# Performance work log

Hardware: AMD Instinct MI355X
Metric: run time of the kernel (lower is better)

The kernel has to match this reference:

```python
import jax, jax.numpy as jnp
import numpy as np

N, E = 50000, 800000
IN, HID, OUT = 256, 128, 128


def setup_inputs() -> dict:
    key = jax.random.key(0)
    ks = jax.random.split(key, 6)
    x = jax.random.normal(ks[0], (N, IN), dtype=jnp.float32)
    edge_index = jax.random.randint(ks[1], (2, E), 0, N, dtype=jnp.int32)
    # xavier_normal-ish scales (exact init values irrelevant for correctness baseline)
    W1 = jax.random.normal(ks[2], (IN, HID), dtype=jnp.float32) * (1.414 / np.sqrt(IN))
    att_src = jax.random.normal(ks[3], (HID,), dtype=jnp.float32) * 0.1
    att_dst = jax.random.normal(ks[4], (HID,), dtype=jnp.float32) * 0.1
    W2 = jax.random.normal(ks[5], (HID, OUT), dtype=jnp.float32) * (1.414 / np.sqrt(HID))
    return {"x": x, "edge_index": edge_index, "W1": W1,
            "att_src": att_src, "att_dst": att_dst, "W2": W2}


def _gat_layer(x, edge_index, W, a_src, a_dst):
    """GATConv(heads=1, concat=False, add_self_loops=False, dropout=0), attention=True."""
    n = x.shape[0]
    src, dst = edge_index[0], edge_index[1]  # message x_j = h[src], grouped by index = dst
    h = x @ W                                 # (N, C)
    e_src = h @ a_src                         # (N,) per-node attention logits
    e_dst = h @ a_dst                         # (N,)
    # per-edge: sigmoid(alpha_j + alpha_i), then scatter-softmax over dst neighborhoods
    alpha = jax.nn.sigmoid(e_src[src] + e_dst[dst])             # (E,)
    m = jax.ops.segment_max(alpha, dst, num_segments=n)          # stable softmax max
    ex = jnp.exp(alpha - m[dst])
    denom = jax.ops.segment_sum(ex, dst, num_segments=n)
    w = ex / denom[dst]                                          # (E,)
    # scatter-add aggregation of weighted source features; heads=1 so mean over heads is identity
    return jax.ops.segment_sum(h[src] * w[:, None], dst, num_segments=n)  # (N, C)


def reference(x, edge_index, W1, att_src, att_dst, W2):
    h1 = jax.nn.elu(_gat_layer(x, edge_index, W1, att_src, att_dst))
    # conv2 called with attention=False: mm(h1, W2).view(N,1,C).mean(1) == plain linear
    return h1 @ W2
```

## Files before the change

### kernel.cpp

```cpp
#include <hip/hip_runtime.h>
#include <hip/hip_bf16.h>

#define N_NODES 50000
#define N_EDGES 800000
#define DIN 256
#define DHID 128
#define DOUT 128
#define NBUCK 196
#define BINBLK 256
#define EPB 3125
#define G1TILES 391

typedef __attribute__((ext_vector_type(8))) short bf16x8;
typedef __attribute__((ext_vector_type(4))) float f32x4;

__device__ inline unsigned short f2b(float f) {
    __hip_bfloat16 b = __float2bfloat16(f);
    return *reinterpret_cast<unsigned short*>(&b);
}

__global__ __launch_bounds__(1024) void convW_lhist_kernel(
    const float* __restrict__ W1, const float* __restrict__ W2,
    const int* __restrict__ ei,
    unsigned short* __restrict__ W1t, unsigned short* __restrict__ W2t,
    int* __restrict__ blockHist)
{
    __shared__ int h[NBUCK];
    const int blk = blockIdx.x;
    const int tid = threadIdx.x;

    if (blk < 48) {
        int i = blk * 1024 + tid;
        if (i < DIN * DHID) {
            int n = i >> 8, k = i & 255;
            int kt = k >> 5, q = (k >> 3) & 3, e = k & 7;
            int t = n >> 4, m = n & 15;
            W1t[(((kt * 8 + t) * 64) + (q * 16 + m)) * 8 + e] = f2b(W1[k * DHID + n]);
        } else {
            int j = i - DIN * DHID;
            int n = j >> 7, k = j & 127;
            int kt = k >> 5, q = (k >> 3) & 3, e = k & 7;
            int t = n >> 4, m = n & 15;
            W2t[(((kt * 8 + t) * 64) + (q * 16 + m)) * 8 + e] = f2b(W2[k * DOUT + n]);
        }
        return;
    }

    const int b = blk - 48;
    if (tid < NBUCK) h[tid] = 0;
    __syncthreads();
    const int base = b * EPB;
    #pragma unroll 1
    for (int it = 0; it < 4; ++it) {
        int e = base + it * 1024 + tid;
        if (e < base + EPB)
            atomicAdd(&h[ei[N_EDGES + e] >> 8], 1);
    }
    __syncthreads();
    if (tid < NBUCK) blockHist[tid * 256 + b] = h[tid];
}

__global__ __launch_bounds__(256) void gemm1_scan_kernel(
    const float* __restrict__ x,
    const unsigned short* __restrict__ W1t,
    const float* __restrict__ att_src,
    const float* __restrict__ att_dst,
    const int* __restrict__ blockHist,
    unsigned short* __restrict__ hb,
    float* __restrict__ es,
    float* __restrict__ ed,
    int* __restrict__ matrixScan)
{
    __shared__ int bs[256];
    __shared__ int sc[256];
    const int tid = threadIdx.x;

    if (blockIdx.x >= G1TILES) {
        const int b = blockIdx.x - G1TILES;

        int tot = 0;
        if (tid < NBUCK) {
            const int* row = blockHist + tid * 256;
            #pragma unroll 4
            for (int i = 0; i < 256; ++i) tot += row[i];
        }
        bs[tid] = tot;
        __syncthreads();
        #pragma unroll
        for (int off = 1; off < 256; off <<= 1) {
            int u = (tid >= off) ? bs[tid - off] : 0;
            __syncthreads();
            bs[tid] += u;
            __syncthreads();
        }
        const int base = (b == 0) ? 0 : bs[b - 1];

        int c = blockHist[b * 256 + tid];
        sc[tid] = c;
        __syncthreads();
        #pragma unroll
        for (int off = 1; off < 256; off <<= 1) {
            int u = (tid >= off) ? sc[tid - off] : 0;
            __syncthreads();
            sc[tid] += u;
            __syncthreads();
        }
        matrixScan[b * 256 + tid] = base + sc[tid] - c;
        return;
    }

    const int wave = tid >> 6, lane = tid & 63;
    const int row0 = blockIdx.x * 128 + wave * 32;
    const int m = lane & 15, q = lane >> 4;

    int r0 = row0 + m;
    int r1 = row0 + 16 + m;
    int rc0 = (r0 < N_NODES) ? r0 : 0;
    int rc1 = (r1 < N_NODES) ? r1 : 0;

    f32x4 acc0[8], acc1[8];
    #pragma unroll
    for (int t = 0; t < 8; ++t) {
        acc0[t] = (f32x4){0.f, 0.f, 0.f, 0.f};
        acc1[t] = (f32x4){0.f, 0.f, 0.f, 0.f};
    }

    const float* xr0 = x + (size_t)rc0 * DIN + q * 8;
    const float* xr1 = x + (size_t)rc1 * DIN + q * 8;
    const short* wb  = (const short*)W1t + lane * 8;

    #pragma unroll
    for (int kt = 0; kt < 8; ++kt) {
        float4 f0 = *(const float4*)(xr0 + kt * 32);
        float4 f1 = *(const float4*)(xr0 + kt * 32 + 4);
        float4 g0 = *(const float4*)(xr1 + kt * 32);
        float4 g1 = *(const float4*)(xr1 + kt * 32 + 4);
        bf16x8 a0, a1;
        a0[0] = (short)f2b(f0.x); a0[1] = (short)f2b(f0.y);
        a0[2] = (short)f2b(f0.z); a0[3] = (short)f2b(f0.w);
        a0[4] = (short)f2b(f1.x); a0[5] = (short)f2b(f1.y);
        a0[6] = (short)f2b(f1.z); a0[7] = (short)f2b(f1.w);
        a1[0] = (short)f2b(g0.x); a1[1] = (short)f2b(g0.y);
        a1[2] = (short)f2b(g0.z); a1[3] = (short)f2b(g0.w);
        a1[4] = (short)f2b(g1.x); a1[5] = (short)f2b(g1.y);
        a1[6] = (short)f2b(g1.z); a1[7] = (short)f2b(g1.w);
        #pragma unroll
        for (int t = 0; t < 8; ++t) {
            bf16x8 b = *(const bf16x8*)(wb + (kt * 8 + t) * 512);
            acc0[t] = __builtin_amdgcn_mfma_f32_16x16x32_bf16(a0, b, acc0[t], 0, 0, 0);
            acc1[t] = __builtin_amdgcn_mfma_f32_16x16x32_bf16(a1, b, acc1[t], 0, 0, 0);
        }
    }

    #pragma unroll
    for (int reg = 0; reg < 4; ++reg) {
        int ra = row0 + q * 4 + reg;
        int rb = row0 + 16 + q * 4 + reg;
        if (ra < N_NODES) {
            #pragma unroll
            for (int t = 0; t < 8; ++t)
                hb[(size_t)ra * DHID + t * 16 + m] = f2b(acc0[t][reg]);
        }
        if (rb < N_NODES) {
            #pragma unroll
            for (int t = 0; t < 8; ++t)
                hb[(size_t)rb * DHID + t * 16 + m] = f2b(acc1[t][reg]);
        }
    }

    float es0[4] = {0,0,0,0}, ed0[4] = {0,0,0,0};
    float es1[4] = {0,0,0,0}, ed1[4] = {0,0,0,0};
    #pragma unroll
    for (int t = 0; t < 8; ++t) {
        float as = att_src[t * 16 + m];
        float ad = att_dst[t * 16 + m];
        #pragma unroll
        for (int reg = 0; reg < 4; ++reg) {
            es0[reg] += acc0[t][reg] * as;
            ed0[reg] += acc0[t][reg] * ad;
            es1[reg] += acc1[t][reg] * as;
            ed1[reg] += acc1[t][reg] * ad;
        }
    }
    #pragma unroll
    for (int off = 8; off; off >>= 1)
        #pragma unroll
        for (int reg = 0; reg < 4; ++reg) {
            es0[reg] += __shfl_xor(es0[reg], off);
            ed0[reg] += __shfl_xor(ed0[reg], off);
            es1[reg] += __shfl_xor(es1[reg], off);
            ed1[reg] += __shfl_xor(ed1[reg], off);
        }
    if (m == 0) {
        #pragma unroll
        for (int reg = 0; reg < 4; ++reg) {
            int ra = row0 + q * 4 + reg;
            int rb = row0 + 16 + q * 4 + reg;
            if (ra < N_NODES) { es[ra] = es0[reg]; ed[ra] = ed0[reg]; }
            if (rb < N_NODES) { es[rb] = es1[reg]; ed[rb] = ed1[reg]; }
        }
    }
}

__global__ __launch_bounds__(1024) void binpass_kernel(
    const int* __restrict__ ei,
    const float* __restrict__ es,
    const float* __restrict__ ed,
    const int* __restrict__ matrixScan,
    int2* __restrict__ binned)
{
    __shared__ int lcur[NBUCK];
    const int t = threadIdx.x, blk = blockIdx.x;
    if (t < NBUCK) lcur[t] = matrixScan[t * 256 + blk];
    __syncthreads();
    const int base = blk * EPB;
    #pragma unroll 1
    for (int it = 0; it < 4; ++it) {
        int e = base + it * 1024 + t;
        if (e < base + EPB) {
            int s = ei[e];
            int d = ei[N_EDGES + e];
            float a  = es[s] + ed[d];
            float sg = 1.f / (1.f + __expf(-a));
            float w  = __expf(sg);
            int pos = atomicAdd(&lcur[d >> 8], 1);
            binned[pos] = make_int2(s | ((d & 255) << 16), __float_as_int(w));
        }
    }
}

__global__ __launch_bounds__(1024) void sortpass_kernel(
    const int2* __restrict__ binned,
    const int* __restrict__ matrixScan,
    int2* __restrict__ sortedSW,
    int* __restrict__ offset,
    int* __restrict__ count)
{
    __shared__ int lhist[256], lscan[256], lcur[256];
    const int t = threadIdx.x, b = blockIdx.x;
    const int start = matrixScan[b * 256];
    const int end   = (b == NBUCK - 1) ? N_EDGES : matrixScan[(b + 1) * 256];
    const int cnt   = end - start;

    if (t < 256) lhist[t] = 0;
    __syncthreads();
    for (int i = t; i < cnt; i += 1024)
        atomicAdd(&lhist[(binned[start + i].x >> 16) & 255], 1);
    __syncthreads();

    int v = 0;
    if (t < 256) { v = lhist[t]; lscan[t] = v; }
    __syncthreads();
    #pragma unroll
    for (int off = 1; off < 256; off <<= 1) {
        int u = 0;
        if (t < 256 && t >= off) u = lscan[t - off];
        __syncthreads();
        if (t < 256) lscan[t] += u;
        __syncthreads();
    }
    if (t < 256) {
        int excl = lscan[t] - v;
        int node = (b << 8) + t;
        if (node < N_NODES) { offset[node] = start + excl; count[node] = v; }
        lcur[t] = excl;
    }
    __syncthreads();

    for (int i = t; i < cnt; i += 1024) {
        int2 ent = binned[start + i];
        int dlow = (ent.x >> 16) & 255;
        int pos = atomicAdd(&lcur[dlow], 1);
        sortedSW[start + pos] = make_int2(ent.x & 0xFFFF, ent.y);
    }
}

__global__ __launch_bounds__(256) void agg_kernel(
    const int2* __restrict__ sortedSW,
    const int* __restrict__ offset,
    const int* __restrict__ count,
    const unsigned short* __restrict__ hb,
    unsigned int* __restrict__ h1b)
{
    int node = (blockIdx.x * 256 + threadIdx.x) >> 6;
    int lane = threadIdx.x & 63;
    if (node >= N_NODES) return;

    int beg = offset[node];
    int deg = count[node];

    float2 acc = make_float2(0.f, 0.f);
    float wsum = 0.f;

    for (int base = 0; base < deg; base += 64) {
        int cnt = min(64, deg - base);
        int2 sw = (lane < cnt) ? sortedSW[beg + base + lane] : make_int2(0, 0);
        int j = 0;

#define TIER(T)                                                                 \
        for (; j + T <= cnt; j += T) {                                          \
            unsigned uu[T]; float ww[T];                                        \
            _Pragma("unroll")                                                   \
            for (int k = 0; k < T; ++k) {                                       \
                int s_ = __builtin_amdgcn_readlane(sw.x, j + k);                \
                uu[k] = *(const unsigned*)(hb + (size_t)s_ * DHID + 2 * lane);  \
            }                                                                   \
            _Pragma("unroll")                                                   \
            for (int k = 0; k < T; ++k)                                         \
                ww[k] = __uint_as_float(                                        \
                    (unsigned)__builtin_amdgcn_readlane(sw.y, j + k));          \
            _Pragma("unroll")                                                   \
            for (int k = 0; k < T; ++k) {                                       \
                wsum  += ww[k];                                                 \
                acc.x += ww[k] * __uint_as_float(uu[k] << 16);                  \
                acc.y += ww[k] * __uint_as_float(uu[k] & 0xffff0000u);          \
            }                                                                   \
        }

        TIER(8)
        TIER(4)
#undef TIER
        for (; j < cnt; ++j) {
            int   sj = __builtin_amdgcn_readlane(sw.x, j);
            float wj = __uint_as_float((unsigned)__builtin_amdgcn_readlane(sw.y, j));
            unsigned u = *(const unsigned*)(hb + (size_t)sj * DHID + 2 * lane);
            acc.x += wj * __uint_as_float(u << 16);
            acc.y += wj * __uint_as_float(u & 0xffff0000u);
            wsum  += wj;
        }
    }
    float inv = (deg > 0) ? 1.f / wsum : 0.f;
    float v0 = acc.x * inv, v1 = acc.y * inv;
    float e0 = v0 > 0.f ? v0 : (__expf(v0) - 1.f);
    float e1 = v1 > 0.f ? v1 : (__expf(v1) - 1.f);
    h1b[(size_t)node * (DHID / 2) + lane] =
        (unsigned)f2b(e0) | ((unsigned)f2b(e1) << 16);
}

__global__ __launch_bounds__(256) void gemm2_mfma(
    const unsigned short* __restrict__ h1b,
    const unsigned short* __restrict__ W2t,
    float* __restrict__ out)
{
    const int tid = threadIdx.x;
    const int wave = tid >> 6, lane = tid & 63;
    const int row0 = blockIdx.x * 128 + wave * 32;
    const int m = lane & 15, q = lane >> 4;

    int r0 = row0 + m;
    int r1 = row0 + 16 + m;
    int rc0 = (r0 < N_NODES) ? r0 : 0;
    int rc1 = (r1 < N_NODES) ? r1 : 0;

    f32x4 acc0[8], acc1[8];
    #pragma unroll
    for (int t = 0; t < 8; ++t) {
        acc0[t] = (f32x4){0.f, 0.f, 0.f, 0.f};
        acc1[t] = (f32x4){0.f, 0.f, 0.f, 0.f};
    }

    const short* xp0 = (const short*)h1b + (size_t)rc0 * DHID + q * 8;
    const short* xp1 = (const short*)h1b + (size_t)rc1 * DHID + q * 8;
    const short* wb  = (const short*)W2t + lane * 8;

    #pragma unroll
    for (int kt = 0; kt < 4; ++kt) {
        bf16x8 a0 = *(const bf16x8*)(xp0 + kt * 32);
        bf16x8 a1 = *(const bf16x8*)(xp1 + kt * 32);
        #pragma unroll
        for (int t = 0; t < 8; ++t) {
            bf16x8 b = *(const bf16x8*)(wb + (kt * 8 + t) * 512);
            acc0[t] = __builtin_amdgcn_mfma_f32_16x16x32_bf16(a0, b, acc0[t], 0, 0, 0);
            acc1[t] = __builtin_amdgcn_mfma_f32_16x16x32_bf16(a1, b, acc1[t], 0, 0, 0);
        }
    }

    #pragma unroll
    for (int reg = 0; reg < 4; ++reg) {
        int ra = row0 + q * 4 + reg;
        int rb = row0 + 16 + q * 4 + reg;
        if (ra < N_NODES) {
            #pragma unroll
            for (int t = 0; t < 8; ++t)
                out[(size_t)ra * DOUT + t * 16 + m] = acc0[t][reg];
        }
        if (rb < N_NODES) {
            #pragma unroll
            for (int t = 0; t < 8; ++t)
                out[(size_t)rb * DOUT + t * 16 + m] = acc1[t][reg];
        }
    }
}

extern "C" void kernel_launch(void* const* d_in, const int* in_sizes, int n_in,
                              void* d_out, int out_size, void* d_ws, size_t ws_size,
                              hipStream_t stream)
{
    const float* x    = (const float*)d_in[0];
    const int*   ei   = (const int*)d_in[1];
    const float* W1   = (const float*)d_in[2];
    const float* asrc = (const float*)d_in[3];
    const float* adst = (const float*)d_in[4];
    const float* W2   = (const float*)d_in[5];
    float*       out  = (float*)d_out;

    char* p = (char*)d_ws;
    unsigned short* hb  = (unsigned short*)p;  p += (size_t)N_NODES * DHID * 2;
    unsigned int*   h1b = (unsigned int*)p;    p += (size_t)N_NODES * DHID * 2;
    unsigned short* W1t = (unsigned short*)p;  p += (size_t)DHID * DIN * 2;
    unsigned short* W2t = (unsigned short*)p;  p += (size_t)DOUT * DHID * 2;
    float* es     = (float*)p;  p += (size_t)N_NODES * 4;
    float* ed     = (float*)p;  p += (size_t)N_NODES * 4;
    int*   offset = (int*)p;    p += (size_t)N_NODES * 4;
    int*   count  = (int*)p;    p += (size_t)N_NODES * 4;
    int*   blockHist    = (int*)p; p += (size_t)NBUCK * 256 * 4;
    int*   matrixScan   = (int*)p; p += (size_t)NBUCK * 256 * 4;
    int2*  binned   = (int2*)p; p += (size_t)N_EDGES * 8;
    int2*  sortedSW = (int2*)p; p += (size_t)N_EDGES * 8;

    convW_lhist_kernel<<<48 + BINBLK, 1024, 0, stream>>>(W1, W2, ei, W1t, W2t, blockHist);

    gemm1_scan_kernel<<<G1TILES + NBUCK, 256, 0, stream>>>(
        x, W1t, asrc, adst, blockHist, hb, es, ed, matrixScan);

    binpass_kernel  <<<BINBLK, 1024, 0, stream>>>(ei, es, ed, matrixScan, binned);
    sortpass_kernel <<<NBUCK, 1024, 0, stream>>>(binned, matrixScan, sortedSW, offset, count);
    agg_kernel<<<(N_NODES * 64 + 255) / 256, 256, 0, stream>>>(
        sortedSW, offset, count, hb, h1b);
    gemm2_mfma<<<G1TILES, 256, 0, stream>>>((const unsigned short*)h1b, W2t, out);
}
```

Measured before the change: 186.7 us.

## Bucket edges by dst low byte and fuse aggregation, ELU and GEMM2 per bucket

Edges are now bucketed by the low 8 bits of the destination, so each of 256 blocks owns a strided set of about 196 nodes. The separate sort pass, aggregation kernel and GEMM2 kernel are replaced by one kernel. It accumulates weighted source features into an LDS tile with shared-memory float atomics, then normalises, applies ELU and runs the MFMA GEMM2 straight from LDS. This removes the second sort pass, the sortedSW, offset and count buffers, and the h1 round trip through global memory. In exchange it relies on LDS atomics and launches only 256 large blocks with about 108KB of LDS each, which may limit parallelism and cause atomic contention.

```diff
diff --git a/kernel.cpp b/kernel.cpp
--- a/kernel.cpp
+++ b/kernel.cpp
@@ -6,7 +6,9 @@
 #define DIN 256
 #define DHID 128
 #define DOUT 128
-#define NBUCK 196
+#define NBUCK 256
+#define NROW 208
+#define LDW 129
 #define BINBLK 256
 #define EPB 3125
 #define G1TILES 391
@@ -54,7 +56,7 @@
     for (int it = 0; it < 4; ++it) {
         int e = base + it * 1024 + tid;
         if (e < base + EPB)
-            atomicAdd(&h[ei[N_EDGES + e] >> 8], 1);
+            atomicAdd(&h[ei[N_EDGES + e] & 255], 1);
     }
     __syncthreads();
     if (tid < NBUCK) blockHist[tid * 256 + b] = h[tid];
@@ -79,7 +81,7 @@
         const int b = blockIdx.x - G1TILES;
 
         int tot = 0;
-        if (tid < NBUCK) {
+        {
             const int* row = blockHist + tid * 256;
             #pragma unroll 4
             for (int i = 0; i < 256; ++i) tot += row[i];
@@ -223,171 +225,116 @@
             float a  = es[s] + ed[d];
             float sg = 1.f / (1.f + __expf(-a));
             float w  = __expf(sg);
-            int pos = atomicAdd(&lcur[d >> 8], 1);
-            binned[pos] = make_int2(s | ((d & 255) << 16), __float_as_int(w));
-        }
-    }
-}
-
-__global__ __launch_bounds__(1024) void sortpass_kernel(
+            int pos = atomicAdd(&lcur[d & 255], 1);
+            binned[pos] = make_int2(s | ((d >> 8) << 16), __float_as_int(w));
+        }
+    }
+}
+
+__global__ __launch_bounds__(1024) void bucketagg_kernel(
     const int2* __restrict__ binned,
     const int* __restrict__ matrixScan,
-    int2* __restrict__ sortedSW,
-    int* __restrict__ offset,
-    int* __restrict__ count)
-{
-    __shared__ int lhist[256], lscan[256], lcur[256];
-    const int t = threadIdx.x, b = blockIdx.x;
+    const unsigned short* __restrict__ hb,
+    const unsigned short* __restrict__ W2t,
+    float* __restrict__ out)
+{
+    __shared__ float acc[NROW * LDW];
+    __shared__ float wsm[NROW];
+    const int tid = threadIdx.x;
+    const int b = blockIdx.x;
+    const int wv = tid >> 6, lane = tid & 63;
+
+    #pragma unroll 4
+    for (int i = tid; i < NROW * LDW; i += 1024) acc[i] = 0.f;
+    if (tid < NROW) wsm[tid] = 0.f;
+    __syncthreads();
+
     const int start = matrixScan[b * 256];
     const int end   = (b == NBUCK - 1) ? N_EDGES : matrixScan[(b + 1) * 256];
-    const int cnt   = end - start;
-
-    if (t < 256) lhist[t] = 0;
-    __syncthreads();
-    for (int i = t; i < cnt; i += 1024)
-        atomicAdd(&lhist[(binned[start + i].x >> 16) & 255], 1);
-    __syncthreads();
-
-    int v = 0;
-    if (t < 256) { v = lhist[t]; lscan[t] = v; }
-    __syncthreads();
-    #pragma unroll
-    for (int off = 1; off < 256; off <<= 1) {
-        int u = 0;
-        if (t < 256 && t >= off) u = lscan[t - off];
-        __syncthreads();
-        if (t < 256) lscan[t] += u;
-        __syncthreads();
-    }
-    if (t < 256) {
-        int excl = lscan[t] - v;
-        int node = (b << 8) + t;
-        if (node < N_NODES) { offset[node] = start + excl; count[node] = v; }
-        lcur[t] = excl;
-    }
-    __syncthreads();
-
-    for (int i = t; i < cnt; i += 1024) {
-        int2 ent = binned[start + i];
-        int dlow = (ent.x >> 16) & 255;
-        int pos = atomicAdd(&lcur[dlow], 1);
-        sortedSW[start + pos] = make_int2(ent.x & 0xFFFF, ent.y);
-    }
-}
-
-__global__ __launch_bounds__(256) void agg_kernel(
-    const int2* __restrict__ sortedSW,
-    const int* __restrict__ offset,
-    const int* __restrict__ count,
-    const unsigned short* __restrict__ hb,
-    unsigned int* __restrict__ h1b)
-{
-    int node = (blockIdx.x * 256 + threadIdx.x) >> 6;
-    int lane = threadIdx.x & 63;
-    if (node >= N_NODES) return;
-
-    int beg = offset[node];
-    int deg = count[node];
-
-    float2 acc = make_float2(0.f, 0.f);
-    float wsum = 0.f;
-
-    for (int base = 0; base < deg; base += 64) {
-        int cnt = min(64, deg - base);
-        int2 sw = (lane < cnt) ? sortedSW[beg + base + lane] : make_int2(0, 0);
+
+    for (int i = start + wv * 64; i < end; i += 1024) {
+        int cnt = min(64, end - i);
+        int2 sw = (lane < cnt) ? binned[i + lane] : make_int2(0, 0);
         int j = 0;
 
-#define TIER(T)                                                                 \
-        for (; j + T <= cnt; j += T) {                                          \
-            unsigned uu[T]; float ww[T];                                        \
-            _Pragma("unroll")                                                   \
-            for (int k = 0; k < T; ++k) {                                       \
-                int s_ = __builtin_amdgcn_readlane(sw.x, j + k);                \
-                uu[k] = *(const unsigned*)(hb + (size_t)s_ * DHID + 2 * lane);  \
-            }                                                                   \
-            _Pragma("unroll")                                                   \
-            for (int k = 0; k < T; ++k)                                         \
-                ww[k] = __uint_as_float(                                        \
-                    (unsigned)__builtin_amdgcn_readlane(sw.y, j + k));          \
-            _Pragma("unroll")                                                   \
-            for (int k = 0; k < T; ++k) {                                       \
-                wsum  += ww[k];                                                 \
-                acc.x += ww[k] * __uint_as_float(uu[k] << 16);                  \
-                acc.y += ww[k] * __uint_as_float(uu[k] & 0xffff0000u);          \
-            }                                                                   \
+#define TIER(T)                                                                  \
+        for (; j + T <= cnt; j += T) {                                           \
+            unsigned uu[T]; float ww[T]; int dl[T];                              \
+            _Pragma("unroll")                                                    \
+            for (int k = 0; k < T; ++k) {                                        \
+                int ex = __builtin_amdgcn_readlane(sw.x, j + k);                 \
+                int s_ = ex & 0xFFFF;                                            \
+                dl[k] = ex >> 16;                                                \
+                uu[k] = *(const unsigned*)(hb + (size_t)s_ * DHID + 2 * lane);   \
+            }                                                                    \
+            _Pragma("unroll")                                                    \
+            for (int k = 0; k < T; ++k)                                          \
+                ww[k] = __uint_as_float(                                         \
+                    (unsigned)__builtin_amdgcn_readlane(sw.y, j + k));           \
+            _Pragma("unroll")                                                    \
+            for (int k = 0; k < T; ++k) {                                        \
+                float* row = acc + dl[k] * LDW + 2 * lane;                       \
+                atomicAdd(row,     ww[k] * __uint_as_float(uu[k] << 16));        \
+                atomicAdd(row + 1, ww[k] * __uint_as_float(uu[k] & 0xffff0000u));\
+                if (lane == 0) atomicAdd(&wsm[dl[k]], ww[k]);                    \
+            }                                                                    \
         }
 
         TIER(8)
         TIER(4)
 #undef TIER
         for (; j < cnt; ++j) {
-            int   sj = __builtin_amdgcn_readlane(sw.x, j);
+            int   ex = __builtin_amdgcn_readlane(sw.x, j);
+            int   s_ = ex & 0xFFFF;
+            int   dlj = ex >> 16;
             float wj = __uint_as_float((unsigned)__builtin_amdgcn_readlane(sw.y, j));
-            unsigned u = *(const unsigned*)(hb + (size_t)sj * DHID + 2 * lane);
-            acc.x += wj * __uint_as_float(u << 16);
-            acc.y += wj * __uint_as_float(u & 0xffff0000u);
-            wsum  += wj;
-        }
-    }
-    float inv = (deg > 0) ? 1.f / wsum : 0.f;
-    float v0 = acc.x * inv, v1 = acc.y * inv;
-    float e0 = v0 > 0.f ? v0 : (__expf(v0) - 1.f);
-    float e1 = v1 > 0.f ? v1 : (__expf(v1) - 1.f);
-    h1b[(size_t)node * (DHID / 2) + lane] =
-        (unsigned)f2b(e0) | ((unsigned)f2b(e1) << 16);
-}
-
-__global__ __launch_bounds__(256) void gemm2_mfma(
-    const unsigned short* __restrict__ h1b,
-    const unsigned short* __restrict__ W2t,
-    float* __restrict__ out)
-{
-    const int tid = threadIdx.x;
-    const int wave = tid >> 6, lane = tid & 63;
-    const int row0 = blockIdx.x * 128 + wave * 32;
+            unsigned u = *(const unsigned*)(hb + (size_t)s_ * DHID + 2 * lane);
+            float* row = acc + dlj * LDW + 2 * lane;
+            atomicAdd(row,     wj * __uint_as_float(u << 16));
+            atomicAdd(row + 1, wj * __uint_as_float(u & 0xffff0000u));
+            if (lane == 0) atomicAdd(&wsm[dlj], wj);
+        }
+    }
+    __syncthreads();
+
+    if (wv > 12) return;
     const int m = lane & 15, q = lane >> 4;
-
-    int r0 = row0 + m;
-    int r1 = row0 + 16 + m;
-    int rc0 = (r0 < N_NODES) ? r0 : 0;
-    int rc1 = (r1 < N_NODES) ? r1 : 0;
-
-    f32x4 acc0[8], acc1[8];
-    #pragma unroll
-    for (int t = 0; t < 8; ++t) {
-        acc0[t] = (f32x4){0.f, 0.f, 0.f, 0.f};
-        acc1[t] = (f32x4){0.f, 0.f, 0.f, 0.f};
-    }
-
-    const short* xp0 = (const short*)h1b + (size_t)rc0 * DHID + q * 8;
-    const short* xp1 = (const short*)h1b + (size_t)rc1 * DHID + q * 8;
-    const short* wb  = (const short*)W2t + lane * 8;
+    const int arow = wv * 16 + m;
+
+    float ws  = wsm[arow];
+    float inv = (ws > 0.f) ? 1.f / ws : 0.f;
+
+    f32x4 c[8];
+    #pragma unroll
+    for (int t = 0; t < 8; ++t) c[t] = (f32x4){0.f, 0.f, 0.f, 0.f};
+
+    const short* wb = (const short*)W2t + lane * 8;
+    const float* ar = acc + arow * LDW + q * 8;
 
     #pragma unroll
     for (int kt = 0; kt < 4; ++kt) {
-        bf16x8 a0 = *(const bf16x8*)(xp0 + kt * 32);
-        bf16x8 a1 = *(const bf16x8*)(xp1 + kt * 32);
+        bf16x8 a;
+        #pragma unroll
+        for (int e = 0; e < 8; ++e) {
+            float v = ar[kt * 32 + e] * inv;
+            float el = v > 0.f ? v : (__expf(v) - 1.f);
+            a[e] = (short)f2b(el);
+        }
         #pragma unroll
         for (int t = 0; t < 8; ++t) {
-            bf16x8 b = *(const bf16x8*)(wb + (kt * 8 + t) * 512);
-            acc0[t] = __builtin_amdgcn_mfma_f32_16x16x32_bf16(a0, b, acc0[t], 0, 0, 0);
-            acc1[t] = __builtin_amdgcn_mfma_f32_16x16x32_bf16(a1, b, acc1[t], 0, 0, 0);
+            bf16x8 bfr = *(const bf16x8*)(wb + (kt * 8 + t) * 512);
+            c[t] = __builtin_amdgcn_mfma_f32_16x16x32_bf16(a, bfr, c[t], 0, 0, 0);
         }
     }
 
     #pragma unroll
     for (int reg = 0; reg < 4; ++reg) {
-        int ra = row0 + q * 4 + reg;
-        int rb = row0 + 16 + q * 4 + reg;
-        if (ra < N_NODES) {
+        int dlow = wv * 16 + q * 4 + reg;
+        int node = (dlow << 8) | b;
+        if (node < N_NODES) {
             #pragma unroll
             for (int t = 0; t < 8; ++t)
-                out[(size_t)ra * DOUT + t * 16 + m] = acc0[t][reg];
-        }
-        if (rb < N_NODES) {
-            #pragma unroll
-            for (int t = 0; t < 8; ++t)
-                out[(size_t)rb * DOUT + t * 16 + m] = acc1[t][reg];
+                out[(size_t)node * DOUT + t * 16 + m] = c[t][reg];
         }
     }
 }
@@ -406,26 +353,21 @@
 
     char* p = (char*)d_ws;
     unsigned short* hb  = (unsigned short*)p;  p += (size_t)N_NODES * DHID * 2;
-    unsigned int*   h1b = (unsigned int*)p;    p += (size_t)N_NODES * DHID * 2;
     unsigned short* W1t = (unsigned short*)p;  p += (size_t)DHID * DIN * 2;
     unsigned short* W2t = (unsigned short*)p;  p += (size_t)DOUT * DHID * 2;
     float* es     = (float*)p;  p += (size_t)N_NODES * 4;
     float* ed     = (float*)p;  p += (size_t)N_NODES * 4;
-    int*   offset = (int*)p;    p += (size_t)N_NODES * 4;
-    int*   count  = (int*)p;    p += (size_t)N_NODES * 4;
     int*   blockHist    = (int*)p; p += (size_t)NBUCK * 256 * 4;
     int*   matrixScan   = (int*)p; p += (size_t)NBUCK * 256 * 4;
     int2*  binned   = (int2*)p; p += (size_t)N_EDGES * 8;
-    int2*  sortedSW = (int2*)p; p += (size_t)N_EDGES * 8;
 
     convW_lhist_kernel<<<48 + BINBLK, 1024, 0, stream>>>(W1, W2, ei, W1t, W2t, blockHist);
 
     gemm1_scan_kernel<<<G1TILES + NBUCK, 256, 0, stream>>>(
         x, W1t, asrc, adst, blockHist, hb, es, ed, matrixScan);
 
-    binpass_kernel  <<<BINBLK, 1024, 0, stream>>>(ei, es, ed, matrixScan, binned);
-    sortpass_kernel <<<NBUCK, 1024, 0, stream>>>(binned, matrixScan, sortedSW, offset, count);
-    agg_kernel<<<(N_NODES * 64 + 255) / 256, 256, 0, stream>>>(
-        sortedSW, offset, count, hb, h1b);
-    gemm2_mfma<<<G1TILES, 256, 0, stream>>>((const unsigned short*)h1b, W2t, out);
-}
+    binpass_kernel<<<BINBLK, 1024, 0, stream>>>(ei, es, ed, matrixScan, binned);
+
+    bucketagg_kernel<<<NBUCK, 1024, 0, stream>>>(
+        binned, matrixScan, hb, W2t, out);
+}
```

Result: slower. 680.5 us (+264.6%).
